# Kernel tuning notes

Measured on AMD Instinct MI355X. Metric: run time of the kernel, lower is better.

Reference implementation:

```python
import jax, jax.numpy as jnp
import numpy as np

B, N, D, D_OUT = 4, 512, 48, 48

def setup_inputs() -> dict:
    key = jax.random.key(0)
    ks = jax.random.split(key, 7)
    s1 = 1.0 / np.sqrt(2 * D)
    s2 = 1.0 / np.sqrt(2 * D)
    s3 = 1.0 / np.sqrt(D)
    return {
        "x": jax.random.normal(ks[0], (B, N, D), dtype=jnp.float32),
        "W1": jax.random.uniform(ks[1], (2 * D, 2 * D), jnp.float32, -s1, s1),
        "b1": jax.random.uniform(ks[2], (2 * D,), jnp.float32, -s1, s1),
        "W2": jax.random.uniform(ks[3], (2 * D, D), jnp.float32, -s2, s2),
        "b2": jax.random.uniform(ks[4], (D,), jnp.float32, -s2, s2),
        "W3": jax.random.uniform(ks[5], (D, D_OUT), jnp.float32, -s3, s3),
        "b3": jax.random.uniform(ks[6], (D_OUT,), jnp.float32, -s3, s3),
    }

def reference(x, W1, b1, W2, b2, W3, b3):
    # x: [B, N, D]
    Bn, Nn, Dn = x.shape
    xi = jnp.broadcast_to(x[:, :, None, :], (Bn, Nn, Nn, Dn))  # row i
    xj = jnp.broadcast_to(x[:, None, :, :], (Bn, Nn, Nn, Dn))  # col j
    pair = jnp.concatenate([xi, xj], axis=-1)  # [B,N,N,2D]
    h = jax.nn.gelu(pair @ W1 + b1, approximate=False)
    h = jax.nn.gelu(h @ W2 + b2, approximate=False)
    pair_out = h @ W3 + b3  # [B,N,N,d_out]
    mask = jnp.triu(jnp.ones((Nn, Nn), dtype=bool), 1)  # j > i masked
    pair_out = jnp.where(mask[None, :, :, None], 0.0, pair_out)
    w = jnp.linalg.norm(pair_out, axis=-1)  # [B,N,N]
    w = jnp.where(mask[None, :, :], -1e9, w)
    w = jax.nn.softmax(w, axis=-1)
    return jnp.einsum('bnj,bnjd->bnd', w, pair_out)
```

## Files before the change

kernel.cpp:

```cpp
#include <hip/hip_runtime.h>
#include <hip/hip_bf16.h>


constexpr int BATCH = 4;
constexpr int SEQ   = 512;
constexpr int DIM   = 48;
constexpr int DIM2  = 96;
constexpr int CH    = 64;

constexpr int AW  = 104;
constexpr int WW  = 96;
constexpr int HW  = 72;

constexpr int OFF_SA   = 0;
constexpr int OFF_W2T  = 13312;
constexpr int OFF_SH   = 22528;
constexpr int OFF_SUI  = 31744;
constexpr int LDS_SIZE = 32128;

typedef short short8v __attribute__((ext_vector_type(8)));
typedef float float4v __attribute__((ext_vector_type(4)));
typedef unsigned int uint2v __attribute__((ext_vector_type(2)));

#define MFMA16(a, b, c) __builtin_amdgcn_mfma_f32_16x16x32_bf16(a, b, c, 0, 0, 0)

__device__ __forceinline__ float gelu_tanh(float x) {
    float u = x * x;
    float q = fmaf(0.10294537f, u, 2.3022077f);
    float e = __builtin_amdgcn_exp2f(x * q);
    float r = __builtin_amdgcn_rcpf(e + 1.0f);
    return fmaf(-x, r, x);
}
__device__ __forceinline__ short f2bf1(float v) {
    return (short)((__float_as_uint(v) + 0x8000u) >> 16);
}
__device__ __forceinline__ unsigned pack_bf16x2(float a, float b) {
    unsigned ua = __float_as_uint(a) + 0x8000u;
    unsigned ub = __float_as_uint(b) + 0x8000u;
    return __builtin_amdgcn_perm(ub, ua, 0x07060302u);
}
constexpr float LOG2E = 1.4426950408889634f;

__global__ __launch_bounds__(192) void uv_kernel(
    const float* __restrict__ x, const float* __restrict__ W1,
    const float* __restrict__ b1, float* __restrict__ U, float* __restrict__ V)
{
    __shared__ float sxT[DIM * 4];
    const int t = threadIdx.x;
    const int row0 = blockIdx.x * 4;
    if (t < DIM * 4) {
        int r = t / DIM, m = t - r * DIM;
        sxT[m * 4 + r] = x[(row0 + r) * DIM + m];
    }
    __syncthreads();
    const bool isU = (t < DIM2);
    const int  k   = isU ? t : (t - DIM2);
    const float* Wcol = W1 + (isU ? 0 : DIM * DIM2) + k;
    float binit = isU ? b1[k] : 0.0f;
    float a0 = binit, a1 = binit, a2 = binit, a3 = binit;
    #pragma unroll 8
    for (int m = 0; m < DIM; ++m) {
        float wv = Wcol[m * DIM2];
        const float4 xa = *(const float4*)&sxT[m * 4];
        a0 = fmaf(wv, xa.x, a0); a1 = fmaf(wv, xa.y, a1);
        a2 = fmaf(wv, xa.z, a2); a3 = fmaf(wv, xa.w, a3);
    }
    float* dst = isU ? U : V;
    dst[(row0 + 0) * DIM2 + k] = a0; dst[(row0 + 1) * DIM2 + k] = a1;
    dst[(row0 + 2) * DIM2 + k] = a2; dst[(row0 + 3) * DIM2 + k] = a3;
}

__global__ __launch_bounds__(256, 5) void pair_kernel(
    const float* __restrict__ U, const float* __restrict__ V,
    const float* __restrict__ W2, const float* __restrict__ b2,
    const float* __restrict__ W3, const float* __restrict__ b3,
    float* __restrict__ out)
{
    __shared__ __align__(16) char smem[LDS_SIZE];
    short* sA   = (short*)(smem + OFF_SA);
    short* sW2T = (short*)(smem + OFF_W2T);
    short* sH   = (short*)(smem + OFF_SH);
    float* sUi  = (float*)(smem + OFF_SUI);

    const int t   = threadIdx.x;
    const int bid = blockIdx.x;
    const int b   = bid & (BATCH - 1);
    const int i   = (SEQ - 1) - (bid >> 2);
    const int rowbase = b * SEQ + i;

    const int lane = t & 63;
    const int w    = t >> 6;
    const int col  = lane & 15;
    const int quad = lane >> 4;
    const int qo   = quad * 8;
    const int m4   = w * 16 + col;
    const int rbase = w * 16 + quad * 4;

    for (int idx = t; idx < DIM2 * DIM; idx += 256) {
        int k = idx / DIM, n = idx - k * DIM;
        sW2T[n * WW + k] = f2bf1(W2[idx]);
    }
    for (int idx = t; idx < DIM * DIM; idx += 256) {
        int k = idx / DIM, n = idx - k * DIM;
        sH[n * HW + k] = f2bf1(W3[idx]);
    }
    for (int idx = t; idx < CH * 16; idx += 256)
        sH[(idx >> 4) * HW + 48 + (idx & 15)] = 0;
    if (t < DIM2) sUi[t] = U[rowbase * DIM2 + t];
    __syncthreads();

    const short* w3b = sH + col * HW + qo;
    const short8v w300 = *(const short8v*)(w3b + 0);
    const short8v w301 = *(const short8v*)(w3b + 32);
    const short8v w310 = *(const short8v*)(w3b + 16*HW + 0);
    const short8v w311 = *(const short8v*)(w3b + 16*HW + 32);
    const short8v w320 = *(const short8v*)(w3b + 32*HW + 0);
    const short8v w321 = *(const short8v*)(w3b + 32*HW + 32);
    const float bb20 = b2[col], bb21 = b2[16 + col], bb22 = b2[32 + col];
    const float bb30 = b3[col], bb31 = b3[16 + col], bb32 = b3[32 + col];
    const short* w2b = sW2T + col * WW + qo;
    __syncthreads();

    const int pr = t >> 2;
    const int pq = t & 3;

    float acc0 = 0.f, acc1 = 0.f, acc2 = 0.f;
    float m_run = -1e30f, l_run = 0.0f;

    for (int j0 = 0; j0 + (w << 4) <= i; j0 += CH) {
        const int jmax = i - j0;

        {
            const float* Vb = V + (b * SEQ + j0 + pr) * DIM2 + pq * 24;
            const float* Ub = sUi + pq * 24;
            #pragma unroll
            for (int kk = 0; kk < 3; ++kk) {
                const float4 v0 = *(const float4*)(Vb + kk * 8);
                const float4 v1 = *(const float4*)(Vb + kk * 8 + 4);
                const float4 u0 = *(const float4*)(Ub + kk * 8);
                const float4 u1 = *(const float4*)(Ub + kk * 8 + 4);
                float g0 = gelu_tanh(u0.x + v0.x);
                float g1 = gelu_tanh(u0.y + v0.y);
                float g2 = gelu_tanh(u0.z + v0.z);
                float g3 = gelu_tanh(u0.w + v0.w);
                float g4 = gelu_tanh(u1.x + v1.x);
                float g5 = gelu_tanh(u1.y + v1.y);
                float g6 = gelu_tanh(u1.z + v1.z);
                float g7 = gelu_tanh(u1.w + v1.w);
                uint2v o0, o1;
                o0.x = pack_bf16x2(g0, g1);
                o0.y = pack_bf16x2(g2, g3);
                o1.x = pack_bf16x2(g4, g5);
                o1.y = pack_bf16x2(g6, g7);
                *(uint2v*)&sA[pr * AW + pq * 24 + kk * 8]     = o0;
                *(uint2v*)&sA[pr * AW + pq * 24 + kk * 8 + 4] = o1;
            }
        }

        {
            const short* arow = &sA[m4 * AW + qo];
            short8v a0 = *(const short8v*)(arow + 0);
            short8v a1 = *(const short8v*)(arow + 32);
            short8v a2 = *(const short8v*)(arow + 64);
            float4v c0 = {bb20, bb20, bb20, bb20};
            float4v c1 = {bb21, bb21, bb21, bb21};
            float4v c2 = {bb22, bb22, bb22, bb22};
            c0 = MFMA16(a0, *(const short8v*)(w2b + 0),          c0);
            c0 = MFMA16(a1, *(const short8v*)(w2b + 32),         c0);
            c0 = MFMA16(a2, *(const short8v*)(w2b + 64),         c0);
            c1 = MFMA16(a0, *(const short8v*)(w2b + 16*WW + 0),  c1);
            c1 = MFMA16(a1, *(const short8v*)(w2b + 16*WW + 32), c1);
            c1 = MFMA16(a2, *(const short8v*)(w2b + 16*WW + 64), c1);
            c2 = MFMA16(a0, *(const short8v*)(w2b + 32*WW + 0),  c2);
            c2 = MFMA16(a1, *(const short8v*)(w2b + 32*WW + 32), c2);
            c2 = MFMA16(a2, *(const short8v*)(w2b + 32*WW + 64), c2);
            #pragma unroll
            for (int r = 0; r < 4; ++r) {
                sH[(rbase + r) * HW +  0 + col] = f2bf1(gelu_tanh(c0[r]));
                sH[(rbase + r) * HW + 16 + col] = f2bf1(gelu_tanh(c1[r]));
                sH[(rbase + r) * HW + 32 + col] = f2bf1(gelu_tanh(c2[r]));
            }
        }

        {
            const short* hrw = &sH[m4 * HW + qo];
            short8v h0 = *(const short8v*)(hrw + 0);
            short8v h1 = *(const short8v*)(hrw + 32);
            float4v p0 = {bb30, bb30, bb30, bb30};
            float4v p1 = {bb31, bb31, bb31, bb31};
            float4v p2 = {bb32, bb32, bb32, bb32};
            p0 = MFMA16(h0, w300, p0); p0 = MFMA16(h1, w301, p0);
            p1 = MFMA16(h0, w310, p1); p1 = MFMA16(h1, w311, p1);
            p2 = MFMA16(h0, w320, p2); p2 = MFMA16(h1, w321, p2);
            float vr[4];
            #pragma unroll
            for (int r = 0; r < 4; ++r) {
                float ss = p0[r]*p0[r] + p1[r]*p1[r] + p2[r]*p2[r];
                ss += __shfl_xor(ss, 1);
                ss += __shfl_xor(ss, 2);
                ss += __shfl_xor(ss, 4);
                ss += __shfl_xor(ss, 8);
                vr[r] = (rbase + r <= jmax) ? __builtin_amdgcn_sqrtf(ss) : -1e30f;
            }
            float mloc = fmaxf(fmaxf(vr[0], vr[1]), fmaxf(vr[2], vr[3]));
            mloc = fmaxf(mloc, __shfl_xor(mloc, 16));
            mloc = fmaxf(mloc, __shfl_xor(mloc, 32));
            float newm = fmaxf(m_run, mloc);
            float sc = __builtin_amdgcn_exp2f((m_run - newm) * LOG2E);
            float e0 = __builtin_amdgcn_exp2f((vr[0] - newm) * LOG2E);
            float e1 = __builtin_amdgcn_exp2f((vr[1] - newm) * LOG2E);
            float e2 = __builtin_amdgcn_exp2f((vr[2] - newm) * LOG2E);
            float e3 = __builtin_amdgcn_exp2f((vr[3] - newm) * LOG2E);
            float s = (e0 + e1) + (e2 + e3);
            s += __shfl_xor(s, 16);
            s += __shfl_xor(s, 32);
            l_run = fmaf(l_run, sc, s);
            m_run = newm;
            acc0 *= sc; acc1 *= sc; acc2 *= sc;
            acc0 = fmaf(e0, p0[0], acc0); acc1 = fmaf(e0, p1[0], acc1); acc2 = fmaf(e0, p2[0], acc2);
            acc0 = fmaf(e1, p0[1], acc0); acc1 = fmaf(e1, p1[1], acc1); acc2 = fmaf(e1, p2[1], acc2);
            acc0 = fmaf(e2, p0[2], acc0); acc1 = fmaf(e2, p1[2], acc1); acc2 = fmaf(e2, p2[2], acc2);
            acc0 = fmaf(e3, p0[3], acc0); acc1 = fmaf(e3, p1[3], acc1); acc2 = fmaf(e3, p2[3], acc2);
        }
    }

    acc0 += __shfl_xor(acc0, 16); acc0 += __shfl_xor(acc0, 32);
    acc1 += __shfl_xor(acc1, 16); acc1 += __shfl_xor(acc1, 32);
    acc2 += __shfl_xor(acc2, 16); acc2 += __shfl_xor(acc2, 32);
    float* red = (float*)smem;
    __syncthreads();
    if (lane < 16) {
        red[w * 64 + lane]      = acc0;
        red[w * 64 + 16 + lane] = acc1;
        red[w * 64 + 32 + lane] = acc2;
    }
    if (lane == 0) { red[w * 64 + 48] = m_run; red[w * 64 + 49] = l_run; }
    __syncthreads();
    if (t < DIM) {
        float mm0 = red[48],       mm1 = red[64 + 48];
        float mm2 = red[128 + 48], mm3 = red[192 + 48];
        float M = fmaxf(fmaxf(mm0, mm1), fmaxf(mm2, mm3));
        float f0 = __builtin_amdgcn_exp2f((mm0 - M) * LOG2E);
        float f1 = __builtin_amdgcn_exp2f((mm1 - M) * LOG2E);
        float f2 = __builtin_amdgcn_exp2f((mm2 - M) * LOG2E);
        float f3 = __builtin_amdgcn_exp2f((mm3 - M) * LOG2E);
        float num = f0 * red[t] + f1 * red[64 + t] + f2 * red[128 + t] + f3 * red[192 + t];
        float den = f0 * red[49] + f1 * red[64 + 49] + f2 * red[128 + 49] + f3 * red[192 + 49];
        out[rowbase * DIM + t] = num / den;
    }
}

extern "C" void kernel_launch(void* const* d_in, const int* in_sizes, int n_in,
                              void* d_out, int out_size, void* d_ws, size_t ws_size,
                              hipStream_t stream) {
    const float* x  = (const float*)d_in[0];
    const float* W1 = (const float*)d_in[1];
    const float* b1 = (const float*)d_in[2];
    const float* W2 = (const float*)d_in[3];
    const float* b2 = (const float*)d_in[4];
    const float* W3 = (const float*)d_in[5];
    const float* b3 = (const float*)d_in[6];
    float* out = (float*)d_out;

    float* U = (float*)d_ws;
    float* V = U + BATCH * SEQ * DIM2;

    uv_kernel<<<BATCH * SEQ / 4, 192, 0, stream>>>(x, W1, b1, U, V);
    pair_kernel<<<BATCH * SEQ, 256, 0, stream>>>(U, V, W2, b2, W3, b3, out);
}
```

Measured before the change: 123.2 us.

## Switch pair MLP to fp16 MFMA and hold W2 fragments in registers

Moves the pair kernel's MFMA operands from bf16 to fp16, using packed round-toward-zero conversion (cvt_pkrtz) so the GELU outputs become one 16-byte LDS store instead of two. W2 is staged through the sA buffer once and its nine fragments are loaded into registers. This removes the dedicated W2 LDS region and the per-chunk W2 LDS reads. The launch-bounds occupancy hint drops from 5 to 4 blocks to make room for the extra registers. fp16 has less range than bf16, and round-toward-zero adds a small rounding bias.

```diff
diff --git a/kernel.cpp b/kernel.cpp
--- a/kernel.cpp
+++ b/kernel.cpp
@@ -9,20 +9,19 @@
 constexpr int CH    = 64;
 
 constexpr int AW  = 104;
-constexpr int WW  = 96;
 constexpr int HW  = 72;
 
 constexpr int OFF_SA   = 0;
-constexpr int OFF_W2T  = 13312;
-constexpr int OFF_SH   = 22528;
-constexpr int OFF_SUI  = 31744;
-constexpr int LDS_SIZE = 32128;
-
-typedef short short8v __attribute__((ext_vector_type(8)));
+constexpr int OFF_SH   = 13312;
+constexpr int OFF_SUI  = 22528;
+constexpr int LDS_SIZE = 22912;
+
+typedef _Float16 half8 __attribute__((ext_vector_type(8)));
+typedef __fp16   fp16x2 __attribute__((ext_vector_type(2)));
 typedef float float4v __attribute__((ext_vector_type(4)));
-typedef unsigned int uint2v __attribute__((ext_vector_type(2)));
-
-#define MFMA16(a, b, c) __builtin_amdgcn_mfma_f32_16x16x32_bf16(a, b, c, 0, 0, 0)
+typedef unsigned int uint4vv __attribute__((ext_vector_type(4)));
+
+#define MFMA16F(a, b, c) __builtin_amdgcn_mfma_f32_16x16x32_f16(a, b, c, 0, 0, 0)
 
 __device__ __forceinline__ float gelu_tanh(float x) {
     float u = x * x;
@@ -30,14 +29,6 @@
     float e = __builtin_amdgcn_exp2f(x * q);
     float r = __builtin_amdgcn_rcpf(e + 1.0f);
     return fmaf(-x, r, x);
-}
-__device__ __forceinline__ short f2bf1(float v) {
-    return (short)((__float_as_uint(v) + 0x8000u) >> 16);
-}
-__device__ __forceinline__ unsigned pack_bf16x2(float a, float b) {
-    unsigned ua = __float_as_uint(a) + 0x8000u;
-    unsigned ub = __float_as_uint(b) + 0x8000u;
-    return __builtin_amdgcn_perm(ub, ua, 0x07060302u);
 }
 constexpr float LOG2E = 1.4426950408889634f;
 
@@ -70,17 +61,16 @@
     dst[(row0 + 2) * DIM2 + k] = a2; dst[(row0 + 3) * DIM2 + k] = a3;
 }
 
-__global__ __launch_bounds__(256, 5) void pair_kernel(
+__global__ __launch_bounds__(256, 4) void pair_kernel(
     const float* __restrict__ U, const float* __restrict__ V,
     const float* __restrict__ W2, const float* __restrict__ b2,
     const float* __restrict__ W3, const float* __restrict__ b3,
     float* __restrict__ out)
 {
     __shared__ __align__(16) char smem[LDS_SIZE];
-    short* sA   = (short*)(smem + OFF_SA);
-    short* sW2T = (short*)(smem + OFF_W2T);
-    short* sH   = (short*)(smem + OFF_SH);
-    float* sUi  = (float*)(smem + OFF_SUI);
+    _Float16* sA  = (_Float16*)(smem + OFF_SA);
+    _Float16* sH  = (_Float16*)(smem + OFF_SH);
+    float*    sUi = (float*)(smem + OFF_SUI);
 
     const int t   = threadIdx.x;
     const int bid = blockIdx.x;
@@ -98,27 +88,36 @@
 
     for (int idx = t; idx < DIM2 * DIM; idx += 256) {
         int k = idx / DIM, n = idx - k * DIM;
-        sW2T[n * WW + k] = f2bf1(W2[idx]);
+        sA[n * AW + k] = (_Float16)W2[idx];
     }
     for (int idx = t; idx < DIM * DIM; idx += 256) {
         int k = idx / DIM, n = idx - k * DIM;
-        sH[n * HW + k] = f2bf1(W3[idx]);
+        sH[n * HW + k] = (_Float16)W3[idx];
     }
     for (int idx = t; idx < CH * 16; idx += 256)
-        sH[(idx >> 4) * HW + 48 + (idx & 15)] = 0;
+        sH[(idx >> 4) * HW + 48 + (idx & 15)] = (_Float16)0.0f;
     if (t < DIM2) sUi[t] = U[rowbase * DIM2 + t];
     __syncthreads();
 
-    const short* w3b = sH + col * HW + qo;
-    const short8v w300 = *(const short8v*)(w3b + 0);
-    const short8v w301 = *(const short8v*)(w3b + 32);
-    const short8v w310 = *(const short8v*)(w3b + 16*HW + 0);
-    const short8v w311 = *(const short8v*)(w3b + 16*HW + 32);
-    const short8v w320 = *(const short8v*)(w3b + 32*HW + 0);
-    const short8v w321 = *(const short8v*)(w3b + 32*HW + 32);
+    const _Float16* w2b = sA + col * AW + qo;
+    const half8 w200 = *(const half8*)(w2b + 0);
+    const half8 w201 = *(const half8*)(w2b + 32);
+    const half8 w202 = *(const half8*)(w2b + 64);
+    const half8 w210 = *(const half8*)(w2b + 16*AW + 0);
+    const half8 w211 = *(const half8*)(w2b + 16*AW + 32);
+    const half8 w212 = *(const half8*)(w2b + 16*AW + 64);
+    const half8 w220 = *(const half8*)(w2b + 32*AW + 0);
+    const half8 w221 = *(const half8*)(w2b + 32*AW + 32);
+    const half8 w222 = *(const half8*)(w2b + 32*AW + 64);
+    const _Float16* w3b = sH + col * HW + qo;
+    const half8 w300 = *(const half8*)(w3b + 0);
+    const half8 w301 = *(const half8*)(w3b + 32);
+    const half8 w310 = *(const half8*)(w3b + 16*HW + 0);
+    const half8 w311 = *(const half8*)(w3b + 16*HW + 32);
+    const half8 w320 = *(const half8*)(w3b + 32*HW + 0);
+    const half8 w321 = *(const half8*)(w3b + 32*HW + 32);
     const float bb20 = b2[col], bb21 = b2[16 + col], bb22 = b2[32 + col];
     const float bb30 = b3[col], bb31 = b3[16 + col], bb32 = b3[32 + col];
-    const short* w2b = sW2T + col * WW + qo;
     __syncthreads();
 
     const int pr = t >> 2;
@@ -147,51 +146,44 @@
                 float g5 = gelu_tanh(u1.y + v1.y);
                 float g6 = gelu_tanh(u1.z + v1.z);
                 float g7 = gelu_tanh(u1.w + v1.w);
-                uint2v o0, o1;
-                o0.x = pack_bf16x2(g0, g1);
-                o0.y = pack_bf16x2(g2, g3);
-                o1.x = pack_bf16x2(g4, g5);
-                o1.y = pack_bf16x2(g6, g7);
-                *(uint2v*)&sA[pr * AW + pq * 24 + kk * 8]     = o0;
-                *(uint2v*)&sA[pr * AW + pq * 24 + kk * 8 + 4] = o1;
+                union { fp16x2 h2[4]; uint4vv u4; } o;
+                o.h2[0] = __builtin_amdgcn_cvt_pkrtz(g0, g1);
+                o.h2[1] = __builtin_amdgcn_cvt_pkrtz(g2, g3);
+                o.h2[2] = __builtin_amdgcn_cvt_pkrtz(g4, g5);
+                o.h2[3] = __builtin_amdgcn_cvt_pkrtz(g6, g7);
+                *(uint4vv*)&sA[pr * AW + pq * 24 + kk * 8] = o.u4;
             }
         }
 
         {
-            const short* arow = &sA[m4 * AW + qo];
-            short8v a0 = *(const short8v*)(arow + 0);
-            short8v a1 = *(const short8v*)(arow + 32);
-            short8v a2 = *(const short8v*)(arow + 64);
+            const _Float16* arow = &sA[m4 * AW + qo];
+            half8 a0 = *(const half8*)(arow + 0);
+            half8 a1 = *(const half8*)(arow + 32);
+            half8 a2 = *(const half8*)(arow + 64);
             float4v c0 = {bb20, bb20, bb20, bb20};
             float4v c1 = {bb21, bb21, bb21, bb21};
             float4v c2 = {bb22, bb22, bb22, bb22};
-            c0 = MFMA16(a0, *(const short8v*)(w2b + 0),          c0);
-            c0 = MFMA16(a1, *(const short8v*)(w2b + 32),         c0);
-            c0 = MFMA16(a2, *(const short8v*)(w2b + 64),         c0);
-            c1 = MFMA16(a0, *(const short8v*)(w2b + 16*WW + 0),  c1);
-            c1 = MFMA16(a1, *(const short8v*)(w2b + 16*WW + 32), c1);
-            c1 = MFMA16(a2, *(const short8v*)(w2b + 16*WW + 64), c1);
-            c2 = MFMA16(a0, *(const short8v*)(w2b + 32*WW + 0),  c2);
-            c2 = MFMA16(a1, *(const short8v*)(w2b + 32*WW + 32), c2);
-            c2 = MFMA16(a2, *(const short8v*)(w2b + 32*WW + 64), c2);
+            c0 = MFMA16F(a0, w200, c0); c0 = MFMA16F(a1, w201, c0); c0 = MFMA16F(a2, w202, c0);
+            c1 = MFMA16F(a0, w210, c1); c1 = MFMA16F(a1, w211, c1); c1 = MFMA16F(a2, w212, c1);
+            c2 = MFMA16F(a0, w220, c2); c2 = MFMA16F(a1, w221, c2); c2 = MFMA16F(a2, w222, c2);
             #pragma unroll
             for (int r = 0; r < 4; ++r) {
-                sH[(rbase + r) * HW +  0 + col] = f2bf1(gelu_tanh(c0[r]));
-                sH[(rbase + r) * HW + 16 + col] = f2bf1(gelu_tanh(c1[r]));
-                sH[(rbase + r) * HW + 32 + col] = f2bf1(gelu_tanh(c2[r]));
+                sH[(rbase + r) * HW +  0 + col] = (_Float16)gelu_tanh(c0[r]);
+                sH[(rbase + r) * HW + 16 + col] = (_Float16)gelu_tanh(c1[r]);
+                sH[(rbase + r) * HW + 32 + col] = (_Float16)gelu_tanh(c2[r]);
             }
         }
 
         {
-            const short* hrw = &sH[m4 * HW + qo];
-            short8v h0 = *(const short8v*)(hrw + 0);
-            short8v h1 = *(const short8v*)(hrw + 32);
+            const _Float16* hrw = &sH[m4 * HW + qo];
+            half8 h0 = *(const half8*)(hrw + 0);
+            half8 h1 = *(const half8*)(hrw + 32);
             float4v p0 = {bb30, bb30, bb30, bb30};
             float4v p1 = {bb31, bb31, bb31, bb31};
             float4v p2 = {bb32, bb32, bb32, bb32};
-            p0 = MFMA16(h0, w300, p0); p0 = MFMA16(h1, w301, p0);
-            p1 = MFMA16(h0, w310, p1); p1 = MFMA16(h1, w311, p1);
-            p2 = MFMA16(h0, w320, p2); p2 = MFMA16(h1, w321, p2);
+            p0 = MFMA16F(h0, w300, p0); p0 = MFMA16F(h1, w301, p0);
+            p1 = MFMA16F(h0, w310, p1); p1 = MFMA16F(h1, w311, p1);
+            p2 = MFMA16F(h0, w320, p2); p2 = MFMA16F(h1, w321, p2);
             float vr[4];
             #pragma unroll
             for (int r = 0; r < 4; ++r) {
```

Result: faster. 112.6 us (-8.7%).
